# Kernel tuning notes

Hardware: AMD Instinct MI355X
Metric: run time of the kernel (lower is better)

## Reference

```python
import jax, jax.numpy as jnp
import numpy as np

IN_FEATURES = 8192
OUT_FEATURES = 8192
MAX_STATES = 100
THRESHOLD = MAX_STATES // 2  # 50


def setup_inputs() -> dict:
    key = jax.random.key(0)
    k1, k2, k3, k4 = jax.random.split(key, 4)
    # mimic module init: states = randn*2 + threshold, clamped to [1, max_states]
    synapse_states = jnp.clip(
        jax.random.normal(k1, (OUT_FEATURES, IN_FEATURES), dtype=jnp.float32) * 2.0 + THRESHOLD,
        1.0, float(MAX_STATES))
    spike_input = (jax.random.uniform(k2, (IN_FEATURES,), dtype=jnp.float32) > 0.5).astype(jnp.float32)
    # non-trivial running state so all update paths are exercised
    membrane_potential = jax.random.uniform(k3, (OUT_FEATURES,), dtype=jnp.float32) * 4.0
    adaptive_threshold = jnp.full((OUT_FEATURES,), 5.0, dtype=jnp.float32)
    eligibility_trace = jax.random.uniform(k4, (OUT_FEATURES, IN_FEATURES), dtype=jnp.float32)
    return {
        "spike_input": spike_input,
        "synapse_states": synapse_states,
        "membrane_potential": membrane_potential,
        "adaptive_threshold": adaptive_threshold,
        "eligibility_trace": eligibility_trace,
    }


def reference(spike_input, synapse_states, membrane_potential, adaptive_threshold, eligibility_trace):
    # ternary (here effectively binary 0/1) weights from integer-like synapse states
    w = (synapse_states > THRESHOLD).astype(jnp.float32)  # [O, I]
    x = spike_input.reshape(-1)                           # [I]
    current = w @ x                                       # [O] (x @ w.T flattened)
    # membrane decay + integrate
    v_mem = membrane_potential * 0.9 + current            # [O]
    spikes = (v_mem >= adaptive_threshold).astype(jnp.float32)
    # eligibility trace: decay + outer-product Hebbian term, clamped
    new_trace = jnp.clip(eligibility_trace * 0.8 + jnp.outer(spikes, x), 0.0, 5.0)
    # homeostatic threshold adaptation
    new_threshold = jnp.clip(adaptive_threshold + (spikes - 0.1) * 0.1, 1.0, 20.0)
    # reset membrane where spiked, leaky retain otherwise
    new_membrane = v_mem * (1.0 - spikes) * 0.1
    return spikes, new_membrane, new_threshold, new_trace
```

## Files before the change

### kernel.cpp

```cpp
#include <hip/hip_runtime.h>


constexpr int O_FEAT = 8192;
constexpr int I_FEAT = 8192;
constexpr float STATE_THR = 50.0f;

__global__ __launch_bounds__(256) void snn_fused_kernel(
    const float* __restrict__ x,
    const float* __restrict__ syn,
    const float* __restrict__ mp,
    const float* __restrict__ thr,
    const float* __restrict__ tr,
    float* __restrict__ out)
{
    const int o = blockIdx.x;
    const int t = threadIdx.x;
    const long long rowoff = (long long)o * I_FEAT;

    const float4* __restrict__ x4 = (const float4*)x;
    const float4* __restrict__ s4 = (const float4*)(syn + rowoff);
    const float4* __restrict__ t4 = (const float4*)(tr + rowoff);
    float4* __restrict__ nt4 = (float4*)(out + 3LL * O_FEAT + rowoff);

    float4 xr[8];
    float sum = 0.0f;
#pragma unroll
    for (int j = 0; j < 8; ++j) {
        const int idx = j * 256 + t;
        const float4 xv = x4[idx];
        const float4 sv = s4[idx];
        xr[j] = xv;
        sum += (sv.x > STATE_THR) ? xv.x : 0.0f;
        sum += (sv.y > STATE_THR) ? xv.y : 0.0f;
        sum += (sv.z > STATE_THR) ? xv.z : 0.0f;
        sum += (sv.w > STATE_THR) ? xv.w : 0.0f;
    }

#pragma unroll
    for (int off = 32; off > 0; off >>= 1)
        sum += __shfl_down(sum, off, 64);

    __shared__ float wsum[4];
    __shared__ float sspike;
    const int wave = t >> 6;
    const int lane = t & 63;
    if (lane == 0) wsum[wave] = sum;
    __syncthreads();

    if (t == 0) {
        const float current = ((wsum[0] + wsum[1]) + wsum[2]) + wsum[3];
        const float v_mem = __fadd_rn(__fmul_rn(mp[o], 0.9f), current);
        const float th = thr[o];
        const float s = (v_mem >= th) ? 1.0f : 0.0f;
        out[o] = s;
        out[O_FEAT + o] = __fmul_rn(__fmul_rn(v_mem, 1.0f - s), 0.1f);
        float nth = __fadd_rn(th, __fmul_rn(s - 0.1f, 0.1f));
        nth = fminf(fmaxf(nth, 1.0f), 20.0f);
        out[2 * O_FEAT + o] = nth;
        sspike = s;
    }
    __syncthreads();
    const float s = sspike;

#pragma unroll
    for (int j = 0; j < 8; ++j) {
        const int idx = j * 256 + t;
        const float4 tv = t4[idx];
        const float4 xv = xr[j];
        float4 r;
        r.x = fminf(fmaxf(__fadd_rn(__fmul_rn(tv.x, 0.8f), s * xv.x), 0.0f), 5.0f);
        r.y = fminf(fmaxf(__fadd_rn(__fmul_rn(tv.y, 0.8f), s * xv.y), 0.0f), 5.0f);
        r.z = fminf(fmaxf(__fadd_rn(__fmul_rn(tv.z, 0.8f), s * xv.z), 0.0f), 5.0f);
        r.w = fminf(fmaxf(__fadd_rn(__fmul_rn(tv.w, 0.8f), s * xv.w), 0.0f), 5.0f);
        nt4[idx] = r;
    }
}

extern "C" void kernel_launch(void* const* d_in, const int* in_sizes, int n_in,
                              void* d_out, int out_size, void* d_ws, size_t ws_size,
                              hipStream_t stream) {
    const float* x   = (const float*)d_in[0];
    const float* syn = (const float*)d_in[1];
    const float* mp  = (const float*)d_in[2];
    const float* th  = (const float*)d_in[3];
    const float* tr  = (const float*)d_in[4];
    float* out = (float*)d_out;

    snn_fused_kernel<<<O_FEAT, 256, 0, stream>>>(x, syn, mp, th, tr, out);
}
```

Baseline: 140.9 us.

## Map one wavefront per output row and use nontemporal trace stores

```diff
diff --git a/kernel.cpp b/kernel.cpp
--- a/kernel.cpp
+++ b/kernel.cpp
@@ -5,7 +5,9 @@
 constexpr int I_FEAT = 8192;
 constexpr float STATE_THR = 50.0f;
 
-__global__ __launch_bounds__(256) void snn_fused_kernel(
+typedef float f32x4 __attribute__((ext_vector_type(4)));
+
+__global__ __launch_bounds__(256) void snn_fused_wave(
     const float* __restrict__ x,
     const float* __restrict__ syn,
     const float* __restrict__ mp,
@@ -13,23 +15,21 @@
     const float* __restrict__ tr,
     float* __restrict__ out)
 {
-    const int o = blockIdx.x;
-    const int t = threadIdx.x;
+    const int lane = threadIdx.x & 63;
+    const int o = (blockIdx.x * blockDim.x + threadIdx.x) >> 6;
     const long long rowoff = (long long)o * I_FEAT;
 
-    const float4* __restrict__ x4 = (const float4*)x;
-    const float4* __restrict__ s4 = (const float4*)(syn + rowoff);
-    const float4* __restrict__ t4 = (const float4*)(tr + rowoff);
-    float4* __restrict__ nt4 = (float4*)(out + 3LL * O_FEAT + rowoff);
+    const f32x4* __restrict__ x4 = (const f32x4*)x;
+    const f32x4* __restrict__ s4 = (const f32x4*)(syn + rowoff);
+    const f32x4* __restrict__ t4 = (const f32x4*)(tr + rowoff);
+    f32x4* __restrict__ n4 = (f32x4*)(out + 3LL * O_FEAT + rowoff);
 
-    float4 xr[8];
     float sum = 0.0f;
-#pragma unroll
-    for (int j = 0; j < 8; ++j) {
-        const int idx = j * 256 + t;
-        const float4 xv = x4[idx];
-        const float4 sv = s4[idx];
-        xr[j] = xv;
+#pragma unroll 4
+    for (int j = 0; j < 32; ++j) {
+        const int idx = j * 64 + lane;
+        const f32x4 sv = s4[idx];
+        const f32x4 xv = x4[idx];
         sum += (sv.x > STATE_THR) ? xv.x : 0.0f;
         sum += (sv.y > STATE_THR) ? xv.y : 0.0f;
         sum += (sv.z > STATE_THR) ? xv.z : 0.0f;
@@ -37,42 +37,30 @@
     }
 
 #pragma unroll
-    for (int off = 32; off > 0; off >>= 1)
-        sum += __shfl_down(sum, off, 64);
+    for (int off = 1; off < 64; off <<= 1)
+        sum += __shfl_xor(sum, off, 64);
 
-    __shared__ float wsum[4];
-    __shared__ float sspike;
-    const int wave = t >> 6;
-    const int lane = t & 63;
-    if (lane == 0) wsum[wave] = sum;
-    __syncthreads();
-
-    if (t == 0) {
-        const float current = ((wsum[0] + wsum[1]) + wsum[2]) + wsum[3];
-        const float v_mem = __fadd_rn(__fmul_rn(mp[o], 0.9f), current);
-        const float th = thr[o];
-        const float s = (v_mem >= th) ? 1.0f : 0.0f;
+    const float v_mem = __fadd_rn(__fmul_rn(mp[o], 0.9f), sum);
+    const float th = thr[o];
+    const float s = (v_mem >= th) ? 1.0f : 0.0f;
+    if (lane == 0) {
         out[o] = s;
         out[O_FEAT + o] = __fmul_rn(__fmul_rn(v_mem, 1.0f - s), 0.1f);
         float nth = __fadd_rn(th, __fmul_rn(s - 0.1f, 0.1f));
-        nth = fminf(fmaxf(nth, 1.0f), 20.0f);
-        out[2 * O_FEAT + o] = nth;
-        sspike = s;
+        out[2 * O_FEAT + o] = fminf(fmaxf(nth, 1.0f), 20.0f);
     }
-    __syncthreads();
-    const float s = sspike;
 
-#pragma unroll
-    for (int j = 0; j < 8; ++j) {
-        const int idx = j * 256 + t;
-        const float4 tv = t4[idx];
-        const float4 xv = xr[j];
-        float4 r;
+#pragma unroll 4
+    for (int j = 0; j < 32; ++j) {
+        const int idx = j * 64 + lane;
+        const f32x4 tv = t4[idx];
+        const f32x4 xv = x4[idx];
+        f32x4 r;
         r.x = fminf(fmaxf(__fadd_rn(__fmul_rn(tv.x, 0.8f), s * xv.x), 0.0f), 5.0f);
         r.y = fminf(fmaxf(__fadd_rn(__fmul_rn(tv.y, 0.8f), s * xv.y), 0.0f), 5.0f);
         r.z = fminf(fmaxf(__fadd_rn(__fmul_rn(tv.z, 0.8f), s * xv.z), 0.0f), 5.0f);
         r.w = fminf(fmaxf(__fadd_rn(__fmul_rn(tv.w, 0.8f), s * xv.w), 0.0f), 5.0f);
-        nt4[idx] = r;
+        __builtin_nontemporal_store(r, &n4[idx]);
     }
 }
 
@@ -86,5 +74,5 @@
     const float* tr  = (const float*)d_in[4];
     float* out = (float*)d_out;
 
-    snn_fused_kernel<<<O_FEAT, 256, 0, stream>>>(x, syn, mp, th, tr, out);
+    snn_fused_wave<<<O_FEAT / 4, 256, 0, stream>>>(x, syn, mp, th, tr, out);
 }
```

After: 149.2 us. 1.06x slower.
